# Kernel optimization log

Measured on AMD Instinct MI355X. Metric: run time of the kernel, lower is better.

The kernel has to match this reference:

```python
import jax, jax.numpy as jnp
import numpy as np

B, N, E = 32, 256, 300   # batch, num hyperedges, word emb size
H, K = 256, 8            # nhidden, nhead
MARGIN = 0.2


def setup_inputs() -> dict:
    key = jax.random.key(0)
    ks = jax.random.split(key, 10)
    s_in = 1.0 / np.sqrt(E)
    s_h = 1.0 / np.sqrt(H)
    s_fc = 1.0 / np.sqrt(H * K)
    return {
        'he_anchor': jax.random.normal(ks[0], (B, N, E), jnp.float32),
        'he_pos': jax.random.normal(ks[1], (B, N, E), jnp.float32),
        'he_neg': jax.random.normal(ks[2], (B, N, E), jnp.float32),
        'W_a2h': jax.random.uniform(ks[3], (H, E), jnp.float32, -s_in, s_in),
        'b_a2h': jax.random.uniform(ks[4], (H,), jnp.float32, -s_in, s_in),
        'W_c2h': jax.random.uniform(ks[5], (H, E), jnp.float32, -s_in, s_in),
        'b_c2h': jax.random.uniform(ks[6], (H,), jnp.float32, -s_in, s_in),
        'W_att': jax.random.uniform(ks[7], (K, H), jnp.float32, -s_h, s_h),
        'b_att': jax.random.uniform(ks[8], (K,), jnp.float32, -s_h, s_h),
        'W_fc': jax.random.uniform(ks[9], (1, H * K), jnp.float32, -s_fc, s_fc),
        'b_fc': jnp.zeros((1,), jnp.float32),
    }


def _score(x, y, W_a2h, b_a2h, W_c2h, b_c2h, W_att, b_att, W_fc, b_fc):
    # a2h / c2h projections, then permute to [B, H, N]
    Aa = jnp.transpose(x @ W_a2h.T + b_a2h, (0, 2, 1))  # [B,H,N]
    Ac = jnp.transpose(y @ W_c2h.T + b_c2h, (0, 2, 1))  # [B,H,M]
    # h2att applied to the outer product Aa[b,h,n]*Ac[b,h,m]; fuse into one einsum
    logits = jnp.einsum('bhn,bhm,kh->bknm', Aa, Ac, W_att) + b_att[None, :, None, None]
    b_, k_, n_, m_ = logits.shape
    att = jax.nn.softmax(logits.reshape(b_, k_, n_ * m_), axis=-1).reshape(b_, k_, n_, m_)
    # per-head bilinear aggregation: out[b,k,h] = sum_{n,m} Aa[b,h,n]*att[b,k,n,m]*Ac[b,h,m]
    t = jnp.einsum('bhn,bknm->bkhm', Aa, att)
    out = jnp.einsum('bkhm,bhm->bkh', t, Ac)
    # torch concat order is head-major: [B, K*H]
    out = out.reshape(b_, k_ * H)
    return out @ W_fc.T + b_fc  # [B,1]


def reference(he_anchor, he_pos, he_neg, W_a2h, b_a2h, W_c2h, b_c2h, W_att, b_att, W_fc, b_fc):
    score_p = _score(he_anchor, he_pos, W_a2h, b_a2h, W_c2h, b_c2h, W_att, b_att, W_fc, b_fc)
    score_n = _score(he_anchor, he_neg, W_a2h, b_a2h, W_c2h, b_c2h, W_att, b_att, W_fc, b_fc)
    loss = jnp.mean(jax.nn.relu(score_n - score_p + MARGIN))
    return loss
```

## Files before the change

kernel.cpp:

```cpp
#include <hip/hip_runtime.h>

#define BB 32
#define NN 256
#define EE 300
#define HH 256
#define KK 8
#define MARGINF 0.2f
#define EP 320

typedef __attribute__((ext_vector_type(8))) short bf16x8;
typedef __attribute__((ext_vector_type(4))) float f32x4;
typedef __attribute__((ext_vector_type(16))) float f32x16;

__device__ inline ushort f2bf(float f) {
  unsigned u = __float_as_uint(f);
  u += 0x7fffu + ((u >> 16) & 1u);
  return (ushort)(u >> 16);
}
__device__ inline float bf2f(ushort s) { return __uint_as_float(((unsigned)s) << 16); }
__device__ inline unsigned cvtpk(float lo, float hi) {
  unsigned r;
  asm("v_cvt_pk_bf16_f32 %0, %1, %2" : "=v"(r) : "v"(lo), "v"(hi));
  return r;
}
__device__ inline void gload_lds16(const ushort* g, ushort* l) {
  __builtin_amdgcn_global_load_lds(
      (const __attribute__((address_space(1))) void*)g,
      (__attribute__((address_space(3))) void*)l, 16, 0, 0);
}

__global__ __launch_bounds__(256) void wconv_kernel(
    const float* __restrict__ Wa, const float* __restrict__ Wc,
    ushort* __restrict__ Wt, unsigned* __restrict__ counter)
{
  const int i = blockIdx.x * 256 + threadIdx.x;
  if (i == 0) counter[0] = 0u;
  const int base = i * 4;
  const int w = base / 81920;
  int r = base - w * 81920;
  const int hb = r / 5120; r -= hb * 5120;
  const int ks = r / 512;  r -= ks * 512;
  const int l = r >> 3, jq = r & 7;
  const int h = hb * 16 + (l & 15);
  const int e0 = ks * 32 + (l >> 4) * 8 + jq;
  const float* src = w ? Wc : Wa;
  ushort4 o = {0, 0, 0, 0};
  if (e0 < EE) {
    const float4 v = *(const float4*)&src[h * EE + e0];
    o.x = f2bf(v.x); o.y = f2bf(v.y); o.z = f2bf(v.z); o.w = f2bf(v.w);
  }
  *(ushort4*)&Wt[base] = o;
}

__global__ __launch_bounds__(256, 4) void proj_kernel(
    const float* __restrict__ he_a, const float* __restrict__ he_p,
    const float* __restrict__ he_n, const ushort* __restrict__ Wt,
    const float* __restrict__ b_a2h, const float* __restrict__ b_c2h,
    ushort* __restrict__ AT)
{
  const int z = blockIdx.y;
  const int which = z >> 5;
  const int b = z & 31;
  const int nb = blockIdx.x;
  const int n0 = nb * 32;
  const int tid = threadIdx.x;
  const int wv = tid >> 6;
  const int lane = tid & 63;
  const int col = lane & 15;
  const int quad = lane >> 4;

  const float* X = (which == 0 ? he_a : which == 1 ? he_p : he_n) + (size_t)b * NN * EE;
  const ushort* W = Wt + (size_t)(which == 0 ? 0 : 1) * 81920;
  const float* bias = (which == 0 ? b_a2h : b_c2h);

  __shared__ __align__(16) ushort sX[32][328];
  __shared__ __align__(16) ushort tr[32][264];

  {
    const int row = tid >> 3, seg = tid & 7;
    const float* xr = X + (size_t)(n0 + row) * EE;
#pragma unroll
    for (int q = 0; q < 10; q++) {
      const int jj = seg + 8 * q;
      float4 xv = {0.f, 0.f, 0.f, 0.f};
      if (jj < 75) xv = *(const float4*)&xr[4 * jj];
      uint2 p; p.x = cvtpk(xv.x, xv.y); p.y = cvtpk(xv.z, xv.w);
      *(uint2*)&sX[row][4 * jj] = p;
    }
  }
  __syncthreads();

  f32x4 acc[2][4];
#pragma unroll
  for (int nf = 0; nf < 2; nf++)
#pragma unroll
    for (int mb = 0; mb < 4; mb++) acc[nf][mb] = (f32x4){0.f, 0.f, 0.f, 0.f};

#pragma unroll
  for (int ks = 0; ks < 10; ks++) {
    const int off = 32 * ks + 8 * quad;
    const bf16x8 a0 = *(const bf16x8*)&sX[col][off];
    const bf16x8 a1 = *(const bf16x8*)&sX[16 + col][off];
#pragma unroll
    for (int mb = 0; mb < 4; mb++) {
      const bf16x8 w8 = *(const bf16x8*)&W[(4 * wv + mb) * 5120 + ks * 512 + lane * 8];
      acc[0][mb] = __builtin_amdgcn_mfma_f32_16x16x32_bf16(a0, w8, acc[0][mb], 0, 0, 0);
      acc[1][mb] = __builtin_amdgcn_mfma_f32_16x16x32_bf16(a1, w8, acc[1][mb], 0, 0, 0);
    }
  }

#pragma unroll
  for (int nf = 0; nf < 2; nf++)
#pragma unroll
    for (int mb = 0; mb < 4; mb++) {
      const float bi = bias[64 * wv + 16 * mb + col];
#pragma unroll
      for (int r = 0; r < 4; r++)
        tr[16 * nf + 4 * quad + r][64 * wv + 16 * mb + col] = f2bf(acc[nf][mb][r] + bi);
    }
  __syncthreads();
  {
    ushort* dst = AT + (size_t)(which * BB + b) * (NN * HH) + (size_t)nb * 8192;
#pragma unroll
    for (int it = 0; it < 4; it++) {
      const int c = it * 256 + tid;
      const int row = c & 31, hs = (c >> 5) & 1, hb = c >> 6;
      *(uint4*)&dst[c * 8] = *(const uint4*)&tr[row][hb * 16 + hs * 8];
    }
  }
}

__global__ __launch_bounds__(512, 1) void attn_kernel(
    const ushort* __restrict__ AT, const float* __restrict__ Watt,
    const float* __restrict__ Wfc, const float* __restrict__ bfc,
    float* __restrict__ scoresK, unsigned* __restrict__ counter,
    float* __restrict__ out)
{
  const int d = blockIdx.x;
  const int x = d & 7;
  const int j = d >> 3;
  const int grp = x * 8 + (j & 7);
  const int kp = j >> 3;
  const int which = grp >> 5;
  const int b = grp & 31;
  const int tid = threadIdx.x;
  const int wid = tid >> 6;
  const int kh = wid >> 2;
  const int ws = wid & 3;
  const int lane = tid & 63;

  const ushort* Ta = AT + (size_t)b * (NN * HH);
  const ushort* Tc = AT + (size_t)((1 + which) * BB + b) * (NN * HH);

  __shared__ __align__(16) ushort sB[65536];
  __shared__ __align__(16) ushort wkb[2][256];
  __shared__ __align__(16) ushort wfb[2][256];
  __shared__ float red[16];
  __shared__ unsigned isLast;

#pragma unroll
  for (int it = 0; it < 16; it++) {
    const int off = (wid * 16 + it) * 512;
    gload_lds16(Tc + off + lane * 8, &sB[off]);
  }
  {
    const int h = tid & 255, hd = tid >> 8;
    const int kt = 2 * kp + hd;
    wkb[hd][h] = f2bf(Watt[(size_t)kt * HH + h] * 1.44269504089f);
    wfb[hd][h] = f2bf(Wfc[(size_t)kt * HH + h]);
  }
  __syncthreads();

  const ushort* wkp = wkb[kh];
  const ushort* wfp = wfb[kh];

  float num = 0.f, den = 0.f;

#pragma unroll 1
  for (int si = 0; si < 2; si++) {
    const int s = si ^ kh;
    bf16x8 saf[16], gaf[16];
    {
      const ushort* abase = Ta + (4 * s + ws) * 8192 + lane * 8;
#pragma unroll
      for (int ks = 0; ks < 16; ks++) {
        const bf16x8 a = *(const bf16x8*)&abase[ks * 512];
        const int off = 16 * ks + 8 * (lane >> 5);
        const bf16x8 w8 = *(const bf16x8*)&wkp[off];
        const bf16x8 f8 = *(const bf16x8*)&wfp[off];
        union { bf16x8 v; unsigned u[4]; } sv, gv;
#pragma unroll
        for (int jj = 0; jj < 4; jj++) {
          const float a0 = bf2f((ushort)a[2 * jj]), a1 = bf2f((ushort)a[2 * jj + 1]);
          sv.u[jj] = cvtpk(a0 * bf2f((ushort)w8[2 * jj]), a1 * bf2f((ushort)w8[2 * jj + 1]));
          gv.u[jj] = cvtpk(a0 * bf2f((ushort)f8[2 * jj]), a1 * bf2f((ushort)f8[2 * jj + 1]));
        }
        saf[ks] = sv.v; gaf[ks] = gv.v;
      }
    }

    const int rot = (2 * kh + ws) & 3;
    f32x16 aS0 = {0,0,0,0,0,0,0,0,0,0,0,0,0,0,0,0};
    f32x16 aG0 = {0,0,0,0,0,0,0,0,0,0,0,0,0,0,0,0};
    f32x16 aS1 = {0,0,0,0,0,0,0,0,0,0,0,0,0,0,0,0};
    f32x16 aG1 = {0,0,0,0,0,0,0,0,0,0,0,0,0,0,0,0};

#define CLUSTER(AS, AG, MBASE, PS, PG, DOW)                                    \
    AS = (f32x16){0,0,0,0,0,0,0,0,0,0,0,0,0,0,0,0};                           \
    AG = (f32x16){0,0,0,0,0,0,0,0,0,0,0,0,0,0,0,0};                           \
    __builtin_amdgcn_s_setprio(1);                                             \
    _Pragma("unroll")                                                          \
    for (int ks = 0; ks < 16; ks++) {                                          \
      const bf16x8 bv = *(const bf16x8*)&sB[(MBASE) + ks * 512 + lane * 8];    \
      AS = __builtin_amdgcn_mfma_f32_32x32x16_bf16(saf[ks], bv, AS, 0, 0, 0);  \
      AG = __builtin_amdgcn_mfma_f32_32x32x16_bf16(gaf[ks], bv, AG, 0, 0, 0);  \
      if (DOW) { const float p = exp2f(PS[ks]); den += p; num = fmaf(p, PG[ks], num); } \
    }                                                                          \
    __builtin_amdgcn_s_setprio(0);

    {
      const int mb0 = rot * 16384;
      CLUSTER(aS0, aG0, mb0, aS1, aG1, 0)
      CLUSTER(aS1, aG1, mb0 + 8192, aS0, aG0, 1)
    }
#pragma unroll 1
    for (int mi = 1; mi < 4; mi++) {
      const int mbase = ((mi + rot) & 3) * 16384;
      CLUSTER(aS0, aG0, mbase, aS1, aG1, 1)
      CLUSTER(aS1, aG1, mbase + 8192, aS0, aG0, 1)
    }
#undef CLUSTER
#pragma unroll
    for (int r = 0; r < 16; r++) {
      const float p = exp2f(aS1[r]);
      den += p; num = fmaf(p, aG1[r], num);
    }
  }

#pragma unroll
  for (int off = 32; off >= 1; off >>= 1) {
    num += __shfl_xor(num, off);
    den += __shfl_xor(den, off);
  }
  if (lane == 0) { red[wid] = num; red[8 + wid] = den; }
  __syncthreads();
  if (tid == 0) {
    const float n0 = red[0] + red[1] + red[2] + red[3];
    const float d0 = red[8] + red[9] + red[10] + red[11];
    const float n1 = red[4] + red[5] + red[6] + red[7];
    const float d1 = red[12] + red[13] + red[14] + red[15];
    atomicExch(&scoresK[(2 * kp) * 64 + grp], n0 / d0);
    atomicExch(&scoresK[(2 * kp + 1) * 64 + grp], n1 / d1);
    __threadfence();
    isLast = (atomicAdd(counter, 1u) == 255u) ? 1u : 0u;
  }
  __syncthreads();

  if (isLast && tid < 64) {
    float s = bfc[0];
#pragma unroll
    for (int kk = 0; kk < KK; kk++)
      s += atomicAdd(&scoresK[kk * 64 + tid], 0.0f);
    const float other = __shfl(s, tid + 32);
    float v = 0.f;
    if (tid < 32) v = fmaxf(other - s + MARGINF, 0.f);
#pragma unroll
    for (int off = 32; off >= 1; off >>= 1) v += __shfl_xor(v, off);
    if (tid == 0) out[0] = v * (1.0f / 32.0f);
  }
}

extern "C" void kernel_launch(void* const* d_in, const int* in_sizes, int n_in,
                              void* d_out, int out_size, void* d_ws, size_t ws_size,
                              hipStream_t stream) {
  const float* he_a  = (const float*)d_in[0];
  const float* he_p  = (const float*)d_in[1];
  const float* he_n  = (const float*)d_in[2];
  const float* W_a2h = (const float*)d_in[3];
  const float* b_a2h = (const float*)d_in[4];
  const float* W_c2h = (const float*)d_in[5];
  const float* b_c2h = (const float*)d_in[6];
  const float* W_att = (const float*)d_in[7];
  const float* W_fc  = (const float*)d_in[9];
  const float* b_fc  = (const float*)d_in[10];

  ushort* AT = (ushort*)d_ws;
  float* scoresK = (float*)(AT + (size_t)3 * BB * NN * HH);
  ushort* Wt = (ushort*)(scoresK + 512);
  unsigned* counter = (unsigned*)(Wt + (size_t)2 * HH * EP);
  (void)ws_size; (void)in_sizes; (void)n_in; (void)out_size;

  wconv_kernel<<<160, 256, 0, stream>>>(W_a2h, W_c2h, Wt, counter);
  dim3 pg(8, 96);
  proj_kernel<<<pg, 256, 0, stream>>>(he_a, he_p, he_n, Wt, b_a2h, b_c2h, AT);
  attn_kernel<<<256, 512, 0, stream>>>(AT, W_att, W_fc, b_fc, scoresK, counter, (float*)d_out);
}
```

Before: 135.6 us.

## Process both n-subtiles per LDS B-fragment load to halve shared reads

The attention kernel now packs A-fragments for both n-subtiles up front and issues four MFMAs per B-fragment loaded from LDS, where before it looped over the subtiles and reloaded B each time. This halves LDS traffic per MFMA and doubles the independent MFMA chains that can overlap the exp/accumulate work. It roughly doubles the register footprint for fragments and accumulators, which risks spills or lower occupancy. The rotation over m-blocks changes to eight blocks keyed by warp id, and the projection kernel's launch bounds drop from 4 to 3 blocks per CU.

Measured after the change: 242.1 us. 78.6% more time.

```diff
diff --git a/kernel.cpp b/kernel.cpp
--- a/kernel.cpp
+++ b/kernel.cpp
@@ -52,7 +52,7 @@
   *(ushort4*)&Wt[base] = o;
 }
 
-__global__ __launch_bounds__(256, 4) void proj_kernel(
+__global__ __launch_bounds__(256, 3) void proj_kernel(
     const float* __restrict__ he_a, const float* __restrict__ he_p,
     const float* __restrict__ he_n, const ushort* __restrict__ Wt,
     const float* __restrict__ b_a2h, const float* __restrict__ b_c2h,
@@ -176,65 +176,73 @@
 
   float num = 0.f, den = 0.f;
 
-#pragma unroll 1
-  for (int si = 0; si < 2; si++) {
-    const int s = si ^ kh;
-    bf16x8 saf[16], gaf[16];
-    {
-      const ushort* abase = Ta + (4 * s + ws) * 8192 + lane * 8;
-#pragma unroll
-      for (int ks = 0; ks < 16; ks++) {
-        const bf16x8 a = *(const bf16x8*)&abase[ks * 512];
-        const int off = 16 * ks + 8 * (lane >> 5);
-        const bf16x8 w8 = *(const bf16x8*)&wkp[off];
-        const bf16x8 f8 = *(const bf16x8*)&wfp[off];
-        union { bf16x8 v; unsigned u[4]; } sv, gv;
-#pragma unroll
-        for (int jj = 0; jj < 4; jj++) {
-          const float a0 = bf2f((ushort)a[2 * jj]), a1 = bf2f((ushort)a[2 * jj + 1]);
-          sv.u[jj] = cvtpk(a0 * bf2f((ushort)w8[2 * jj]), a1 * bf2f((ushort)w8[2 * jj + 1]));
-          gv.u[jj] = cvtpk(a0 * bf2f((ushort)f8[2 * jj]), a1 * bf2f((ushort)f8[2 * jj + 1]));
-        }
-        saf[ks] = sv.v; gaf[ks] = gv.v;
-      }
-    }
-
-    const int rot = (2 * kh + ws) & 3;
-    f32x16 aS0 = {0,0,0,0,0,0,0,0,0,0,0,0,0,0,0,0};
-    f32x16 aG0 = {0,0,0,0,0,0,0,0,0,0,0,0,0,0,0,0};
-    f32x16 aS1 = {0,0,0,0,0,0,0,0,0,0,0,0,0,0,0,0};
-    f32x16 aG1 = {0,0,0,0,0,0,0,0,0,0,0,0,0,0,0,0};
-
-#define CLUSTER(AS, AG, MBASE, PS, PG, DOW)                                    \
-    AS = (f32x16){0,0,0,0,0,0,0,0,0,0,0,0,0,0,0,0};                           \
-    AG = (f32x16){0,0,0,0,0,0,0,0,0,0,0,0,0,0,0,0};                           \
+  bf16x8 saf0[16], gaf0[16], saf1[16], gaf1[16];
+#define PACK(SAF, GAF, NBK)                                                    \
+  {                                                                            \
+    const ushort* abase = Ta + (NBK) * 8192 + lane * 8;                        \
+    _Pragma("unroll")                                                          \
+    for (int ks = 0; ks < 16; ks++) {                                          \
+      const bf16x8 a = *(const bf16x8*)&abase[ks * 512];                       \
+      const int off = 16 * ks + 8 * (lane >> 5);                               \
+      const bf16x8 w8 = *(const bf16x8*)&wkp[off];                             \
+      const bf16x8 f8 = *(const bf16x8*)&wfp[off];                             \
+      union { bf16x8 v; unsigned u[4]; } sv, gv;                               \
+      _Pragma("unroll")                                                        \
+      for (int jj = 0; jj < 4; jj++) {                                         \
+        const float a0 = bf2f((ushort)a[2 * jj]), a1 = bf2f((ushort)a[2 * jj + 1]); \
+        sv.u[jj] = cvtpk(a0 * bf2f((ushort)w8[2 * jj]), a1 * bf2f((ushort)w8[2 * jj + 1])); \
+        gv.u[jj] = cvtpk(a0 * bf2f((ushort)f8[2 * jj]), a1 * bf2f((ushort)f8[2 * jj + 1])); \
+      }                                                                        \
+      SAF[ks] = sv.v; GAF[ks] = gv.v;                                          \
+    }                                                                          \
+  }
+  PACK(saf0, gaf0, ws)
+  PACK(saf1, gaf1, 4 + ws)
+#undef PACK
+
+  const int rot = wid;
+  f32x16 aSA0, aGA0, aSA1, aGA1, aSB0, aGB0, aSB1, aGB1;
+
+#define BODY(AS0, AG0, AS1, AG1, MBASE, PS0, PG0, PS1, PG1, DOW)               \
+    AS0 = (f32x16){0,0,0,0,0,0,0,0,0,0,0,0,0,0,0,0};                          \
+    AG0 = (f32x16){0,0,0,0,0,0,0,0,0,0,0,0,0,0,0,0};                          \
+    AS1 = (f32x16){0,0,0,0,0,0,0,0,0,0,0,0,0,0,0,0};                          \
+    AG1 = (f32x16){0,0,0,0,0,0,0,0,0,0,0,0,0,0,0,0};                          \
     __builtin_amdgcn_s_setprio(1);                                             \
     _Pragma("unroll")                                                          \
     for (int ks = 0; ks < 16; ks++) {                                          \
       const bf16x8 bv = *(const bf16x8*)&sB[(MBASE) + ks * 512 + lane * 8];    \
-      AS = __builtin_amdgcn_mfma_f32_32x32x16_bf16(saf[ks], bv, AS, 0, 0, 0);  \
-      AG = __builtin_amdgcn_mfma_f32_32x32x16_bf16(gaf[ks], bv, AG, 0, 0, 0);  \
-      if (DOW) { const float p = exp2f(PS[ks]); den += p; num = fmaf(p, PG[ks], num); } \
+      AS0 = __builtin_amdgcn_mfma_f32_32x32x16_bf16(saf0[ks], bv, AS0, 0, 0, 0);\
+      AG0 = __builtin_amdgcn_mfma_f32_32x32x16_bf16(gaf0[ks], bv, AG0, 0, 0, 0);\
+      AS1 = __builtin_amdgcn_mfma_f32_32x32x16_bf16(saf1[ks], bv, AS1, 0, 0, 0);\
+      AG1 = __builtin_amdgcn_mfma_f32_32x32x16_bf16(gaf1[ks], bv, AG1, 0, 0, 0);\
+      if (DOW) {                                                               \
+        const float p0 = exp2f(PS0[ks]); den += p0; num = fmaf(p0, PG0[ks], num); \
+        const float p1 = exp2f(PS1[ks]); den += p1; num = fmaf(p1, PG1[ks], num); \
+      }                                                                        \
     }                                                                          \
     __builtin_amdgcn_s_setprio(0);
 
-    {
-      const int mb0 = rot * 16384;
-      CLUSTER(aS0, aG0, mb0, aS1, aG1, 0)
-      CLUSTER(aS1, aG1, mb0 + 8192, aS0, aG0, 1)
-    }
+  BODY(aSA0, aGA0, aSA1, aGA1, ((0 + rot) & 7) * 8192,
+       aSB0, aGB0, aSB1, aGB1, 0)
 #pragma unroll 1
-    for (int mi = 1; mi < 4; mi++) {
-      const int mbase = ((mi + rot) & 3) * 16384;
-      CLUSTER(aS0, aG0, mbase, aS1, aG1, 1)
-      CLUSTER(aS1, aG1, mbase + 8192, aS0, aG0, 1)
-    }
-#undef CLUSTER
-#pragma unroll
-    for (int r = 0; r < 16; r++) {
-      const float p = exp2f(aS1[r]);
-      den += p; num = fmaf(p, aG1[r], num);
-    }
+  for (int mi = 0; mi < 3; mi++) {
+    const int m1 = ((2 * mi + 1 + rot) & 7) * 8192;
+    const int m2 = ((2 * mi + 2 + rot) & 7) * 8192;
+    BODY(aSB0, aGB0, aSB1, aGB1, m1, aSA0, aGA0, aSA1, aGA1, 1)
+    BODY(aSA0, aGA0, aSA1, aGA1, m2, aSB0, aGB0, aSB1, aGB1, 1)
+  }
+  {
+    const int m7 = ((7 + rot) & 7) * 8192;
+    BODY(aSB0, aGB0, aSB1, aGB1, m7, aSA0, aGA0, aSA1, aGA1, 1)
+  }
+#undef BODY
+#pragma unroll
+  for (int r = 0; r < 16; r++) {
+    const float p0 = exp2f(aSB0[r]);
+    den += p0; num = fmaf(p0, aGB0[r], num);
+    const float p1 = exp2f(aSB1[r]);
+    den += p1; num = fmaf(p1, aGB1[r], num);
   }
 
 #pragma unroll
```
